# Optimization experiments

Measured on AMD Instinct MI355X. Metric: run time of the kernel, lower is better.

The kernel has to match this reference:

```python
import jax, jax.numpy as jnp
import numpy as np

NUM_HEADS = 12

def _elu1(x):
    return jax.nn.elu(x) + 1.0

def setup_inputs() -> dict:
    key = jax.random.key(0)
    ks = jax.random.split(key, 7)
    B, Nq, Nk, D = 8, 4096, 1024, 768
    s = 0.02
    return {
        "x_query": jax.random.normal(ks[0], (B, Nq, D), dtype=jnp.float32),
        "x_key_value": jax.random.normal(ks[1], (B, Nk, D), dtype=jnp.float32),
        "Wq": jax.random.normal(ks[2], (D, D), dtype=jnp.float32) * s,
        "Wk": jax.random.normal(ks[3], (D, D), dtype=jnp.float32) * s,
        "Wv": jax.random.normal(ks[4], (D, D), dtype=jnp.float32) * s,
        "Wo": jax.random.normal(ks[5], (D, D), dtype=jnp.float32) * s,
        "bo": jax.random.normal(ks[6], (D,), dtype=jnp.float32) * s,
    }

def reference(x_query, x_key_value, Wq, Wk, Wv, Wo, bo):
    B, Nq, D = x_query.shape
    Nk = x_key_value.shape[1]
    H = NUM_HEADS
    hd = D // H
    # projections (torch Linear: x @ W.T), split heads -> [B, H, N, hd]
    q = (x_query @ Wq.T).reshape(B, Nq, H, hd).transpose(0, 2, 1, 3)
    k = (x_key_value @ Wk.T).reshape(B, Nk, H, hd).transpose(0, 2, 1, 3)
    v = (x_key_value @ Wv.T).reshape(B, Nk, H, hd).transpose(0, 2, 1, 3)
    q = _elu1(q)
    k = _elu1(k)
    # kv: [B,H,hd,hd]; k_sum: [B,H,hd]
    kv = jnp.einsum('bhnd,bhne->bhde', k, v)
    k_sum = k.sum(axis=2)
    z = 1.0 / (jnp.einsum('bhqd,bhd->bhq', q, k_sum) + 1e-6)  # [B,H,Nq]
    attn_out = jnp.einsum('bhqd,bhde->bhqe', q, kv) * z[..., None]
    attn_out = attn_out.transpose(0, 2, 1, 3).reshape(B, Nq, D)
    return attn_out @ Wo.T + bo
```

## Files before the change

kernel.cpp:

```cpp
#include <hip/hip_runtime.h>

typedef _Float16 half8_t __attribute__((ext_vector_type(8)));
typedef _Float16 half4_t __attribute__((ext_vector_type(4)));
typedef float    float4_t __attribute__((ext_vector_type(4)));

#define DIM 768

#define GLOAD16(g, l) __builtin_amdgcn_global_load_lds(                        \
    (const __attribute__((address_space(1))) void*)(g),                        \
    (__attribute__((address_space(3))) void*)(l), 16, 0, 0)

__global__ __launch_bounds__(256) void cast_f32_f16(const float* __restrict__ s,
                                                    _Float16* __restrict__ d, int n8)
{
    int i = blockIdx.x * 256 + threadIdx.x;
    if (i < n8) {
        float4_t f0 = *(const float4_t*)&s[(size_t)i * 8];
        float4_t f1 = *(const float4_t*)&s[(size_t)i * 8 + 4];
        half8_t h;
        #pragma unroll
        for (int e = 0; e < 4; ++e) { h[e] = (_Float16)f0[e]; h[e + 4] = (_Float16)f1[e]; }
        *(half8_t*)&d[(size_t)i * 8] = h;
    }
}

__global__ __launch_bounds__(256) void cast4_f32_f16(
    const float* __restrict__ s0, const float* __restrict__ s1,
    const float* __restrict__ s2, const float* __restrict__ s3,
    _Float16* __restrict__ d0, _Float16* __restrict__ d1,
    _Float16* __restrict__ d2, _Float16* __restrict__ d3)
{
    const float* s; _Float16* d;
    switch (blockIdx.y) {
        case 0: s = s0; d = d0; break;
        case 1: s = s1; d = d1; break;
        case 2: s = s2; d = d2; break;
        default: s = s3; d = d3; break;
    }
    int i = blockIdx.x * 256 + threadIdx.x;
    float4_t f0 = *(const float4_t*)&s[(size_t)i * 8];
    float4_t f1 = *(const float4_t*)&s[(size_t)i * 8 + 4];
    half8_t h;
    #pragma unroll
    for (int e = 0; e < 4; ++e) { h[e] = (_Float16)f0[e]; h[e + 4] = (_Float16)f1[e]; }
    *(half8_t*)&d[(size_t)i * 8] = h;
}

template<bool ELU, bool BIAS, bool OUT_F32>
__global__ __launch_bounds__(256) void gemm_h16(const _Float16* __restrict__ A,
                                                const _Float16* __restrict__ W,
                                                const float* __restrict__ bias,
                                                void* __restrict__ Ov)
{
    __shared__ __align__(16) _Float16 As[128 * 64];
    __shared__ __align__(16) _Float16 Bs[128 * 64];

    const int nwg = gridDim.x;
    const int cpx = nwg >> 3;
    const int bid = (blockIdx.x & 7) * cpx + (blockIdx.x >> 3);
    const int brow = bid / 6;
    const int bcol = bid - brow * 6;
    const int row0 = brow * 128, col0 = bcol * 128;

    const int tid  = threadIdx.x;
    const int w    = tid >> 6, lane = tid & 63;
    const int lr   = lane & 15;
    const int lkg  = lane >> 4;
    const int wm   = (w & 1) * 64;
    const int wn   = (w >> 1) * 64;

    const int sr = w * 8 + (lane >> 3);
    const int sc = (lane & 7) * 8;
    const _Float16* Ag = A + (size_t)(row0 + sr) * DIM + sc;
    const _Float16* Wg = W + (size_t)(col0 + sr) * DIM + sc;

    float4_t acc[4][4] = {};

    for (int k0 = 0; k0 < DIM; k0 += 64) {
        #pragma unroll
        for (int j = 0; j < 4; ++j)
            GLOAD16(Ag + k0 + j * 32 * DIM, &As[j * 2048 + w * 512]);
        #pragma unroll
        for (int j = 0; j < 4; ++j)
            GLOAD16(Wg + k0 + j * 32 * DIM, &Bs[j * 2048 + w * 512]);
        __syncthreads();

        half8_t aF[2][4], bF[2][4];
        #pragma unroll
        for (int kk = 0; kk < 2; ++kk) {
            #pragma unroll
            for (int mi = 0; mi < 4; ++mi)
                aF[kk][mi] = *(const half8_t*)&As[(wm + mi * 16 + lr) * 64 + kk * 32 + lkg * 8];
            #pragma unroll
            for (int ni = 0; ni < 4; ++ni)
                bF[kk][ni] = *(const half8_t*)&Bs[(wn + ni * 16 + lr) * 64 + kk * 32 + lkg * 8];
        }
        #pragma unroll
        for (int kk = 0; kk < 2; ++kk)
            #pragma unroll
            for (int mi = 0; mi < 4; ++mi)
                #pragma unroll
                for (int ni = 0; ni < 4; ++ni)
                    acc[mi][ni] = __builtin_amdgcn_mfma_f32_16x16x32_f16(
                        aF[kk][mi], bF[kk][ni], acc[mi][ni], 0, 0, 0);
        __syncthreads();
    }

    #pragma unroll
    for (int mi = 0; mi < 4; ++mi) {
        #pragma unroll
        for (int ni = 0; ni < 4; ++ni) {
            #pragma unroll
            for (int e = 0; e < 4; ++e) {
                int r = row0 + wm + mi * 16 + lkg * 4 + e;
                int c = col0 + wn + ni * 16 + lr;
                float v = acc[mi][ni][e];
                if (ELU) v = (v > 0.0f) ? (v + 1.0f) : __expf(v);
                if (BIAS) v += bias[c];
                if (OUT_F32) ((float*)Ov)[(size_t)r * DIM + c] = v;
                else         ((_Float16*)Ov)[(size_t)r * DIM + c] = (_Float16)v;
            }
        }
    }
}

__global__ __launch_bounds__(256) void kv_reduce(const _Float16* __restrict__ k16,
                                                 const _Float16* __restrict__ v16,
                                                 float* __restrict__ kvh,
                                                 float* __restrict__ ksum)
{
    __shared__ __align__(16) _Float16 K[128][64];
    __shared__ __align__(16) _Float16 V[128][64];
    const int chunk = blockIdx.x;
    const int bh    = blockIdx.y;
    const int b = bh / 12, h = bh % 12;
    const int tid = threadIdx.x;

    const size_t base = ((size_t)b * 1024 + (size_t)chunk * 128) * DIM + h * 64;
    #pragma unroll
    for (int j = 0; j < 4; ++j) {
        int idx = j * 256 + tid;
        int r = idx >> 3, c = (idx & 7) * 8;
        *(half8_t*)&K[r][c] = *(const half8_t*)&k16[base + (size_t)r * DIM + c];
        *(half8_t*)&V[r][c] = *(const half8_t*)&v16[base + (size_t)r * DIM + c];
    }
    __syncthreads();

    const int d0 = (tid & 15) * 4;
    const int e0 = (tid >> 4) * 4;
    float acc[4][4] = {};
    #pragma unroll 4
    for (int n = 0; n < 128; ++n) {
        half4_t kd = *(const half4_t*)&K[n][d0];
        half4_t ve = *(const half4_t*)&V[n][e0];
        #pragma unroll
        for (int i = 0; i < 4; ++i)
            #pragma unroll
            for (int j = 0; j < 4; ++j)
                acc[i][j] += (float)ve[i] * (float)kd[j];
    }
    float* kvp = kvh + (size_t)bh * 64 * 64;
    #pragma unroll
    for (int i = 0; i < 4; ++i)
        #pragma unroll
        for (int j = 0; j < 4; ++j)
            atomicAdd(&kvp[(e0 + i) * 64 + d0 + j], acc[i][j]);

    if (tid < 64) {
        float s = 0.0f;
        for (int n = 0; n < 128; ++n) s += (float)K[n][tid];
        atomicAdd(&ksum[bh * 64 + tid], s);
    }
}

__global__ __launch_bounds__(256) void attn_kernel(_Float16* __restrict__ q16,
                                                   const float* __restrict__ kvh,
                                                   const float* __restrict__ ksum)
{
    __shared__ __align__(16) _Float16 Q[128][72];
    __shared__ __align__(16) _Float16 Bv[64][72];
    __shared__ float S[64];
    __shared__ float Z[128];

    const int h    = blockIdx.x;
    const int rb   = blockIdx.y;
    const int row0 = rb * 128;
    const int b    = row0 >> 12;
    const int bh   = b * 12 + h;
    const int tid  = threadIdx.x;

    #pragma unroll
    for (int j = 0; j < 4; ++j) {
        int idx = j * 256 + tid;
        int r = idx >> 3, c = (idx & 7) * 8;
        *(half8_t*)&Q[r][c] =
            *(const half8_t*)&q16[(size_t)(row0 + r) * DIM + h * 64 + c];
    }
    #pragma unroll
    for (int j = 0; j < 4; ++j) {
        int idx = j * 256 + tid;
        int r = idx >> 4, c = (idx & 15) * 4;
        float4_t f = *(const float4_t*)&kvh[((size_t)bh * 64 + r) * 64 + c];
        half4_t hh;
        #pragma unroll
        for (int e = 0; e < 4; ++e) hh[e] = (_Float16)f[e];
        *(half4_t*)&Bv[r][c] = hh;
    }
    if (tid < 64) S[tid] = ksum[bh * 64 + tid];
    __syncthreads();

    if (tid < 128) {
        float dot = 0.0f;
        #pragma unroll 8
        for (int d = 0; d < 64; ++d) dot += (float)Q[tid][d] * S[d];
        Z[tid] = 1.0f / (dot + 1e-6f);
    }
    __syncthreads();

    const int w = tid >> 6, lane = tid & 63;
    const int lr = lane & 15, lkg = lane >> 4;
    float4_t acc[2][4] = {};
    #pragma unroll
    for (int kc = 0; kc < 2; ++kc) {
        half8_t aF[2], bF[4];
        #pragma unroll
        for (int mi = 0; mi < 2; ++mi)
            aF[mi] = *(const half8_t*)&Q[w * 32 + mi * 16 + lr][kc * 32 + lkg * 8];
        #pragma unroll
        for (int ni = 0; ni < 4; ++ni)
            bF[ni] = *(const half8_t*)&Bv[ni * 16 + lr][kc * 32 + lkg * 8];
        #pragma unroll
        for (int mi = 0; mi < 2; ++mi)
            #pragma unroll
            for (int ni = 0; ni < 4; ++ni)
                acc[mi][ni] = __builtin_amdgcn_mfma_f32_16x16x32_f16(
                    aF[mi], bF[ni], acc[mi][ni], 0, 0, 0);
    }
    #pragma unroll
    for (int mi = 0; mi < 2; ++mi) {
        #pragma unroll
        for (int ni = 0; ni < 4; ++ni) {
            #pragma unroll
            for (int e = 0; e < 4; ++e) {
                int r = w * 32 + mi * 16 + lkg * 4 + e;
                float v = acc[mi][ni][e] * Z[r];
                q16[(size_t)(row0 + r) * DIM + h * 64 + ni * 16 + lr] = (_Float16)v;
            }
        }
    }
}

extern "C" void kernel_launch(void* const* d_in, const int* in_sizes, int n_in,
                              void* d_out, int out_size, void* d_ws, size_t ws_size,
                              hipStream_t stream)
{
    const float* xq  = (const float*)d_in[0];
    const float* xkv = (const float*)d_in[1];
    const float* Wq  = (const float*)d_in[2];
    const float* Wk  = (const float*)d_in[3];
    const float* Wv  = (const float*)d_in[4];
    const float* Wo  = (const float*)d_in[5];
    const float* bo  = (const float*)d_in[6];

    char* ws = (char*)d_ws;
    const size_t SZ_XKV16 = (size_t)8192 * 768 * 2;
    const size_t SZ_Q16   = (size_t)32768 * 768 * 2;
    const size_t SZ_W16   = (size_t)768 * 768 * 2;
    const size_t SZ_KVH   = (size_t)96 * 64 * 64 * 4;
    const size_t SZ_KSUM  = (size_t)96 * 64 * 4;

    _Float16* xkv16 = (_Float16*)(ws);
    _Float16* q16   = (_Float16*)(ws + SZ_XKV16);
    _Float16* Wq16  = (_Float16*)(ws + SZ_XKV16 + SZ_Q16);
    _Float16* Wk16  = (_Float16*)(ws + SZ_XKV16 + SZ_Q16 + SZ_W16);
    _Float16* Wv16  = (_Float16*)(ws + SZ_XKV16 + SZ_Q16 + 2 * SZ_W16);
    _Float16* Wo16  = (_Float16*)(ws + SZ_XKV16 + SZ_Q16 + 3 * SZ_W16);
    float*    kvh   = (float*)   (ws + SZ_XKV16 + SZ_Q16 + 4 * SZ_W16);
    float*    ksum  = (float*)   (ws + SZ_XKV16 + SZ_Q16 + 4 * SZ_W16 + SZ_KVH);

    char* ob = (char*)d_out;
    _Float16* xq16 = (_Float16*)(ob);
    _Float16* k16  = (_Float16*)(ob + 50331648);
    _Float16* v16  = (_Float16*)(ob + 50331648 + 12582912);
    float*    out  = (float*)d_out;

    cast_f32_f16<<<12288, 256, 0, stream>>>(xq,  xq16,  3145728);
    cast_f32_f16<<< 3072, 256, 0, stream>>>(xkv, xkv16,  786432);
    cast4_f32_f16<<<dim3(288, 4), 256, 0, stream>>>(Wq, Wk, Wv, Wo,
                                                    Wq16, Wk16, Wv16, Wo16);
    hipMemsetAsync(kvh, 0, SZ_KVH + SZ_KSUM, stream);

    gemm_h16<true , false, false><<< 384, 256, 0, stream>>>(xkv16, Wk16, nullptr, k16);
    gemm_h16<false, false, false><<< 384, 256, 0, stream>>>(xkv16, Wv16, nullptr, v16);
    gemm_h16<true , false, false><<<1536, 256, 0, stream>>>(xq16 , Wq16, nullptr, q16);

    kv_reduce<<<dim3(8, 96), 256, 0, stream>>>(k16, v16, kvh, ksum);
    attn_kernel<<<dim3(12, 256), 256, 0, stream>>>(q16, kvh, ksum);

    gemm_h16<false, true , true ><<<1536, 256, 0, stream>>>(q16, Wo16, bo, out);
}
```

Baseline: 253.8 us.

## Replace GEMM with 256x128-tile triple-buffered pipelined kernel using swizzled LDS

The fp16 MFMA GEMM moves from 128x128 tiles with 256 threads and a single LDS buffer to 256x128 tiles with 512 threads. Global-to-LDS loads run through a 3-stage ring prefetched two k-steps ahead. LDS addresses use an XOR swizzle to avoid bank conflicts, and split-phase barriers with s_setprio let MFMA work overlap the issue of the next loads. The aim is to hide global load latency and raise MFMA utilisation, at the cost of 144KB of LDS per block (one block per CU) and fewer blocks in the grid.

```diff
diff --git a/kernel.cpp b/kernel.cpp
--- a/kernel.cpp
+++ b/kernel.cpp
@@ -9,6 +9,8 @@
 #define GLOAD16(g, l) __builtin_amdgcn_global_load_lds(                        \
     (const __attribute__((address_space(1))) void*)(g),                        \
     (__attribute__((address_space(3))) void*)(l), 16, 0, 0)
+
+#define MFMA16(a, b, c) __builtin_amdgcn_mfma_f32_16x16x32_f16((a), (b), (c), 0, 0, 0)
 
 __global__ __launch_bounds__(256) void cast_f32_f16(const float* __restrict__ s,
                                                     _Float16* __restrict__ d, int n8)
@@ -47,73 +49,124 @@
 }
 
 template<bool ELU, bool BIAS, bool OUT_F32>
-__global__ __launch_bounds__(256) void gemm_h16(const _Float16* __restrict__ A,
-                                                const _Float16* __restrict__ W,
-                                                const float* __restrict__ bias,
-                                                void* __restrict__ Ov)
-{
-    __shared__ __align__(16) _Float16 As[128 * 64];
-    __shared__ __align__(16) _Float16 Bs[128 * 64];
+__global__ __launch_bounds__(512) void gemm256(const _Float16* __restrict__ A,
+                                               const _Float16* __restrict__ W,
+                                               const float* __restrict__ bias,
+                                               void* __restrict__ Ov)
+{
+    __shared__ __align__(16) _Float16 lds[3 * 24576];
 
     const int nwg = gridDim.x;
     const int cpx = nwg >> 3;
     const int bid = (blockIdx.x & 7) * cpx + (blockIdx.x >> 3);
-    const int brow = bid / 6;
-    const int bcol = bid - brow * 6;
-    const int row0 = brow * 128, col0 = bcol * 128;
+    const int brow = bid / 6, bcol = bid - brow * 6;
+    const int row0 = brow * 256, col0 = bcol * 128;
 
     const int tid  = threadIdx.x;
-    const int w    = tid >> 6, lane = tid & 63;
+    const int wid  = tid >> 6, lane = tid & 63;
+    const int wr   = wid >> 2;
+    const int wc   = wid & 3;
     const int lr   = lane & 15;
     const int lkg  = lane >> 4;
-    const int wm   = (w & 1) * 64;
-    const int wn   = (w >> 1) * 64;
-
-    const int sr = w * 8 + (lane >> 3);
-    const int sc = (lane & 7) * 8;
-    const _Float16* Ag = A + (size_t)(row0 + sr) * DIM + sc;
-    const _Float16* Wg = W + (size_t)(col0 + sr) * DIM + sc;
-
-    float4_t acc[4][4] = {};
-
-    for (int k0 = 0; k0 < DIM; k0 += 64) {
-        #pragma unroll
-        for (int j = 0; j < 4; ++j)
-            GLOAD16(Ag + k0 + j * 32 * DIM, &As[j * 2048 + w * 512]);
-        #pragma unroll
-        for (int j = 0; j < 4; ++j)
-            GLOAD16(Wg + k0 + j * 32 * DIM, &Bs[j * 2048 + w * 512]);
-        __syncthreads();
-
-        half8_t aF[2][4], bF[2][4];
-        #pragma unroll
-        for (int kk = 0; kk < 2; ++kk) {
-            #pragma unroll
-            for (int mi = 0; mi < 4; ++mi)
-                aF[kk][mi] = *(const half8_t*)&As[(wm + mi * 16 + lr) * 64 + kk * 32 + lkg * 8];
-            #pragma unroll
-            for (int ni = 0; ni < 4; ++ni)
-                bF[kk][ni] = *(const half8_t*)&Bs[(wn + ni * 16 + lr) * 64 + kk * 32 + lkg * 8];
-        }
-        #pragma unroll
-        for (int kk = 0; kk < 2; ++kk)
-            #pragma unroll
-            for (int mi = 0; mi < 4; ++mi)
-                #pragma unroll
-                for (int ni = 0; ni < 4; ++ni)
-                    acc[mi][ni] = __builtin_amdgcn_mfma_f32_16x16x32_f16(
-                        aF[kk][mi], bF[kk][ni], acc[mi][ni], 0, 0, 0);
-        __syncthreads();
-    }
-
-    #pragma unroll
-    for (int mi = 0; mi < 4; ++mi) {
-        #pragma unroll
-        for (int ni = 0; ni < 4; ++ni) {
+    const int x    = lr & 7;
+
+    const int  srow = wid * 8 + (lane >> 3);
+    const int  sg   = ((lane & 7) ^ (lane >> 3)) * 8;
+    const _Float16* Ast = A + (size_t)(row0 + srow) * DIM + sg;
+    const _Float16* Bst = W + (size_t)(col0 + srow) * DIM + sg;
+
+#define LDSA(s) (&lds[(s) * 24576])
+#define LDSB(s) (&lds[(s) * 24576 + 16384])
+#define STAGE_A(t, s, j) GLOAD16(Ast + (size_t)(t) * 64 + (size_t)(j) * 64 * DIM, \
+                                 LDSA(s) + (j) * 4096 + wid * 512)
+#define STAGE_B(t, s, j) GLOAD16(Bst + (size_t)(t) * 64 + (size_t)(j) * 64 * DIM, \
+                                 LDSB(s) + (j) * 4096 + wid * 512)
+
+    const int ard = (wr * 128 + lr) * 64;
+    const int brd = (wc * 32 + lr) * 64;
+    const int g0  = (lkg ^ x) * 8;
+    const int g1  = g0 ^ 32;
+
+    float4_t acc[8][2] = {};
+
+    STAGE_A(0, 0, 0); STAGE_A(0, 0, 1); STAGE_A(0, 0, 2); STAGE_A(0, 0, 3);
+    STAGE_B(0, 0, 0); STAGE_B(0, 0, 1);
+    STAGE_A(1, 1, 0); STAGE_A(1, 1, 1); STAGE_A(1, 1, 2); STAGE_A(1, 1, 3);
+    STAGE_B(1, 1, 0); STAGE_B(1, 1, 1);
+    asm volatile("s_waitcnt vmcnt(6)" ::: "memory");
+    __builtin_amdgcn_s_barrier();
+
+    int s = 0, s2 = 2;
+    for (int t = 0; t < 12; ++t) {
+        const _Float16* Asl = LDSA(s);
+        const _Float16* Bsl = LDSB(s);
+        const bool pf = (t < 10);
+
+        half8_t bf[2][2];
+        bf[0][0] = *(const half8_t*)&Bsl[brd + g0];
+        bf[0][1] = *(const half8_t*)&Bsl[brd + g1];
+        bf[1][0] = *(const half8_t*)&Bsl[brd + 1024 + g0];
+        bf[1][1] = *(const half8_t*)&Bsl[brd + 1024 + g1];
+        half8_t af0[4][2];
+        #pragma unroll
+        for (int i = 0; i < 4; ++i) {
+            af0[i][0] = *(const half8_t*)&Asl[ard + i * 1024 + g0];
+            af0[i][1] = *(const half8_t*)&Asl[ard + i * 1024 + g1];
+        }
+        if (pf) { STAGE_A(t + 2, s2, 0); STAGE_A(t + 2, s2, 1); STAGE_A(t + 2, s2, 2); }
+        __builtin_amdgcn_s_barrier();
+        asm volatile("s_waitcnt lgkmcnt(0)" ::: "memory");
+        __builtin_amdgcn_sched_barrier(0);
+        __builtin_amdgcn_s_setprio(1);
+        #pragma unroll
+        for (int i = 0; i < 4; ++i)
+            #pragma unroll
+            for (int ni = 0; ni < 2; ++ni) {
+                acc[i][ni] = MFMA16(af0[i][0], bf[ni][0], acc[i][ni]);
+                acc[i][ni] = MFMA16(af0[i][1], bf[ni][1], acc[i][ni]);
+            }
+        __builtin_amdgcn_s_setprio(0);
+        __builtin_amdgcn_sched_barrier(0);
+        __builtin_amdgcn_s_barrier();
+
+        half8_t af1[4][2];
+        #pragma unroll
+        for (int i = 0; i < 4; ++i) {
+            af1[i][0] = *(const half8_t*)&Asl[ard + 4096 + i * 1024 + g0];
+            af1[i][1] = *(const half8_t*)&Asl[ard + 4096 + i * 1024 + g1];
+        }
+        if (pf) { STAGE_A(t + 2, s2, 3); STAGE_B(t + 2, s2, 0); STAGE_B(t + 2, s2, 1); }
+        __builtin_amdgcn_s_barrier();
+        asm volatile("s_waitcnt lgkmcnt(0)" ::: "memory");
+        __builtin_amdgcn_sched_barrier(0);
+        __builtin_amdgcn_s_setprio(1);
+        #pragma unroll
+        for (int i = 0; i < 4; ++i)
+            #pragma unroll
+            for (int ni = 0; ni < 2; ++ni) {
+                acc[4 + i][ni] = MFMA16(af1[i][0], bf[ni][0], acc[4 + i][ni]);
+                acc[4 + i][ni] = MFMA16(af1[i][1], bf[ni][1], acc[4 + i][ni]);
+            }
+        __builtin_amdgcn_s_setprio(0);
+        __builtin_amdgcn_sched_barrier(0);
+
+        if (t < 11) {
+            if (pf) asm volatile("s_waitcnt vmcnt(6)" ::: "memory");
+            else    asm volatile("s_waitcnt vmcnt(0)" ::: "memory");
+            __builtin_amdgcn_s_barrier();
+        }
+        s  = (s  == 2) ? 0 : s  + 1;
+        s2 = (s2 == 2) ? 0 : s2 + 1;
+    }
+
+    #pragma unroll
+    for (int mi = 0; mi < 8; ++mi) {
+        #pragma unroll
+        for (int ni = 0; ni < 2; ++ni) {
             #pragma unroll
             for (int e = 0; e < 4; ++e) {
-                int r = row0 + wm + mi * 16 + lkg * 4 + e;
-                int c = col0 + wn + ni * 16 + lr;
+                int r = row0 + wr * 128 + mi * 16 + lkg * 4 + e;
+                int c = col0 + wc * 32 + ni * 16 + lr;
                 float v = acc[mi][ni][e];
                 if (ELU) v = (v > 0.0f) ? (v + 1.0f) : __expf(v);
                 if (BIAS) v += bias[c];
@@ -122,6 +175,10 @@
             }
         }
     }
+#undef LDSA
+#undef LDSB
+#undef STAGE_A
+#undef STAGE_B
 }
 
 __global__ __launch_bounds__(256) void kv_reduce(const _Float16* __restrict__ k16,
@@ -233,8 +290,7 @@
         for (int mi = 0; mi < 2; ++mi)
             #pragma unroll
             for (int ni = 0; ni < 4; ++ni)
-                acc[mi][ni] = __builtin_amdgcn_mfma_f32_16x16x32_f16(
-                    aF[mi], bF[ni], acc[mi][ni], 0, 0, 0);
+                acc[mi][ni] = MFMA16(aF[mi], bF[ni], acc[mi][ni]);
     }
     #pragma unroll
     for (int mi = 0; mi < 2; ++mi) {
@@ -290,12 +346,12 @@
                                                     Wq16, Wk16, Wv16, Wo16);
     hipMemsetAsync(kvh, 0, SZ_KVH + SZ_KSUM, stream);
 
-    gemm_h16<true , false, false><<< 384, 256, 0, stream>>>(xkv16, Wk16, nullptr, k16);
-    gemm_h16<false, false, false><<< 384, 256, 0, stream>>>(xkv16, Wv16, nullptr, v16);
-    gemm_h16<true , false, false><<<1536, 256, 0, stream>>>(xq16 , Wq16, nullptr, q16);
+    gemm256<true , false, false><<< 192, 512, 0, stream>>>(xkv16, Wk16, nullptr, k16);
+    gemm256<false, false, false><<< 192, 512, 0, stream>>>(xkv16, Wv16, nullptr, v16);
+    gemm256<true , false, false><<< 768, 512, 0, stream>>>(xq16 , Wq16, nullptr, q16);
 
     kv_reduce<<<dim3(8, 96), 256, 0, stream>>>(k16, v16, kvh, ksum);
     attn_kernel<<<dim3(12, 256), 256, 0, stream>>>(q16, kvh, ksum);
 
-    gemm_h16<false, true , true ><<<1536, 256, 0, stream>>>(q16, Wo16, bo, out);
-}
+    gemm256<false, true , true ><<< 768, 512, 0, stream>>>(q16, Wo16, bo, out);
+}
```

After: 230.6 us. -9.1%, faster.

## Pipeline GEMMs with triple-buffered LDS and fuse Q/K/V projections into one launch

Applied to the files above, without the earlier changes.

Replaces the single-buffered 128x128 GEMM with a 256x128-tile, 512-thread core that uses a three-stage global-to-LDS pipeline with k-steps of 32. It uses partial vmcnt waits, raw barriers and raised wave priority around the MFMA block. The three Q/K/V projection launches merge into one grid that dispatches by block id. The aim is to overlap global loads with MFMA work, cut barrier stalls and launch count, and improve tile reuse. In exchange, LDS use per block rises, and correctness now depends on hand-written waitcnt and sched-barrier ordering.

```diff
diff --git a/kernel.cpp b/kernel.cpp
--- a/kernel.cpp
+++ b/kernel.cpp
@@ -9,6 +9,8 @@
 #define GLOAD16(g, l) __builtin_amdgcn_global_load_lds(                        \
     (const __attribute__((address_space(1))) void*)(g),                        \
     (__attribute__((address_space(3))) void*)(l), 16, 0, 0)
+
+#define MFMA16(a, b, c) __builtin_amdgcn_mfma_f32_16x16x32_f16((a), (b), (c), 0, 0, 0)
 
 __global__ __launch_bounds__(256) void cast_f32_f16(const float* __restrict__ s,
                                                     _Float16* __restrict__ d, int n8)
@@ -46,79 +48,143 @@
     *(half8_t*)&d[(size_t)i * 8] = h;
 }
 
-template<bool ELU, bool BIAS, bool OUT_F32>
-__global__ __launch_bounds__(256) void gemm_h16(const _Float16* __restrict__ A,
-                                                const _Float16* __restrict__ W,
-                                                const float* __restrict__ bias,
-                                                void* __restrict__ Ov)
-{
-    __shared__ __align__(16) _Float16 As[128 * 64];
-    __shared__ __align__(16) _Float16 Bs[128 * 64];
-
-    const int nwg = gridDim.x;
-    const int cpx = nwg >> 3;
-    const int bid = (blockIdx.x & 7) * cpx + (blockIdx.x >> 3);
-    const int brow = bid / 6;
-    const int bcol = bid - brow * 6;
-    const int row0 = brow * 128, col0 = bcol * 128;
-
+__device__ __forceinline__ void gemm_core(const _Float16* __restrict__ A,
+                                          const _Float16* __restrict__ W,
+                                          int row0, int col0, _Float16* lds,
+                                          float4_t acc[4][4])
+{
     const int tid  = threadIdx.x;
-    const int w    = tid >> 6, lane = tid & 63;
-    const int lr   = lane & 15;
-    const int lkg  = lane >> 4;
-    const int wm   = (w & 1) * 64;
-    const int wn   = (w >> 1) * 64;
-
-    const int sr = w * 8 + (lane >> 3);
-    const int sc = (lane & 7) * 8;
-    const _Float16* Ag = A + (size_t)(row0 + sr) * DIM + sc;
-    const _Float16* Wg = W + (size_t)(col0 + sr) * DIM + sc;
+    const int wid  = tid >> 6, lane = tid & 63;
+    const int wr   = wid >> 1;
+    const int wc   = wid & 1;
+
+    const int srow  = lane & 15;
+    const int skoct = lane >> 4;
+    const _Float16* As0 = A + (size_t)(row0 + wid * 32 + srow)      * DIM + skoct * 8;
+    const _Float16* As1 = A + (size_t)(row0 + wid * 32 + 16 + srow) * DIM + skoct * 8;
+    const _Float16* Bs0 = W + (size_t)(col0 + wid * 16 + srow)      * DIM + skoct * 8;
+
+#define STAGE(t, s) do {                                                      \
+        GLOAD16(As0 + (t) * 32, &lds[(s) * 12288 + (2 * wid) * 512]);         \
+        GLOAD16(As1 + (t) * 32, &lds[(s) * 12288 + (2 * wid + 1) * 512]);     \
+        GLOAD16(Bs0 + (t) * 32, &lds[(s) * 12288 + 8192 + wid * 512]);        \
+    } while (0)
+
+    const int aoff = (wr * 4) * 512 + lane * 8;
+    const int boff = 8192 + (wc * 4) * 512 + lane * 8;
+
+    STAGE(0, 0);
+    STAGE(1, 1);
+    asm volatile("s_waitcnt vmcnt(3)" ::: "memory");
+    __builtin_amdgcn_s_barrier();
+    __builtin_amdgcn_sched_barrier(0);
+
+    int s = 0, s2 = 2;
+    for (int t = 0; t < 24; ++t) {
+        const _Float16* sl = &lds[s * 12288];
+        half8_t af[4], bf[4];
+        #pragma unroll
+        for (int mi = 0; mi < 4; ++mi)
+            af[mi] = *(const half8_t*)&sl[aoff + mi * 512];
+        #pragma unroll
+        for (int ni = 0; ni < 4; ++ni)
+            bf[ni] = *(const half8_t*)&sl[boff + ni * 512];
+        if (t < 22) STAGE(t + 2, s2);
+
+        __builtin_amdgcn_s_setprio(1);
+        #pragma unroll
+        for (int mi = 0; mi < 4; ++mi)
+            #pragma unroll
+            for (int ni = 0; ni < 4; ++ni)
+                acc[mi][ni] = MFMA16(af[mi], bf[ni], acc[mi][ni]);
+        __builtin_amdgcn_s_setprio(0);
+
+        if (t < 23) {
+            __builtin_amdgcn_sched_barrier(0);
+            if (t < 22) asm volatile("s_waitcnt vmcnt(3)" ::: "memory");
+            else        asm volatile("s_waitcnt vmcnt(0)" ::: "memory");
+            __builtin_amdgcn_s_barrier();
+            __builtin_amdgcn_sched_barrier(0);
+        }
+        s  = (s  == 2) ? 0 : s  + 1;
+        s2 = (s2 == 2) ? 0 : s2 + 1;
+    }
+#undef STAGE
+}
+
+__global__ __launch_bounds__(512, 4) void proj_qkv(
+    const _Float16* __restrict__ xq16, const _Float16* __restrict__ xkv16,
+    const _Float16* __restrict__ Wq16, const _Float16* __restrict__ Wk16,
+    const _Float16* __restrict__ Wv16,
+    _Float16* __restrict__ q16, _Float16* __restrict__ k16,
+    _Float16* __restrict__ v16)
+{
+    __shared__ __align__(16) _Float16 lds[3 * 12288];
+
+    const int cpx = gridDim.x >> 3;
+    int bid = (blockIdx.x & 7) * cpx + (blockIdx.x >> 3);
+
+    const _Float16 *A, *W;
+    _Float16 *O;
+    bool elu;
+    int brow, bcol;
+    if (bid < 768) {
+        A = xq16; W = Wq16; O = q16; elu = true;
+        brow = bid / 6; bcol = bid - brow * 6;
+    } else {
+        int u = bid - 768;
+        int mat = u / 192;  u -= mat * 192;
+        A = xkv16; W = mat ? Wv16 : Wk16; O = mat ? v16 : k16; elu = !mat;
+        brow = u / 6; bcol = u - brow * 6;
+    }
+    const int row0 = brow * 256, col0 = bcol * 128;
 
     float4_t acc[4][4] = {};
-
-    for (int k0 = 0; k0 < DIM; k0 += 64) {
-        #pragma unroll
-        for (int j = 0; j < 4; ++j)
-            GLOAD16(Ag + k0 + j * 32 * DIM, &As[j * 2048 + w * 512]);
-        #pragma unroll
-        for (int j = 0; j < 4; ++j)
-            GLOAD16(Wg + k0 + j * 32 * DIM, &Bs[j * 2048 + w * 512]);
-        __syncthreads();
-
-        half8_t aF[2][4], bF[2][4];
-        #pragma unroll
-        for (int kk = 0; kk < 2; ++kk) {
-            #pragma unroll
-            for (int mi = 0; mi < 4; ++mi)
-                aF[kk][mi] = *(const half8_t*)&As[(wm + mi * 16 + lr) * 64 + kk * 32 + lkg * 8];
-            #pragma unroll
-            for (int ni = 0; ni < 4; ++ni)
-                bF[kk][ni] = *(const half8_t*)&Bs[(wn + ni * 16 + lr) * 64 + kk * 32 + lkg * 8];
+    gemm_core(A, W, row0, col0, lds, acc);
+
+    const int wid = threadIdx.x >> 6, lane = threadIdx.x & 63;
+    const int wr = wid >> 1, wc = wid & 1, lr = lane & 15, lkg = lane >> 4;
+    #pragma unroll
+    for (int mi = 0; mi < 4; ++mi) {
+        #pragma unroll
+        for (int ni = 0; ni < 4; ++ni) {
+            #pragma unroll
+            for (int e = 0; e < 4; ++e) {
+                int r = row0 + wr * 64 + mi * 16 + lkg * 4 + e;
+                int c = col0 + wc * 64 + ni * 16 + lr;
+                float v = acc[mi][ni][e];
+                if (elu) v = (v > 0.0f) ? (v + 1.0f) : __expf(v);
+                O[(size_t)r * DIM + c] = (_Float16)v;
+            }
         }
-        #pragma unroll
-        for (int kk = 0; kk < 2; ++kk)
-            #pragma unroll
-            for (int mi = 0; mi < 4; ++mi)
-                #pragma unroll
-                for (int ni = 0; ni < 4; ++ni)
-                    acc[mi][ni] = __builtin_amdgcn_mfma_f32_16x16x32_f16(
-                        aF[kk][mi], bF[kk][ni], acc[mi][ni], 0, 0, 0);
-        __syncthreads();
-    }
-
+    }
+}
+
+__global__ __launch_bounds__(512, 4) void out_proj(
+    const _Float16* __restrict__ a16, const _Float16* __restrict__ Wo16,
+    const float* __restrict__ bo, float* __restrict__ out)
+{
+    __shared__ __align__(16) _Float16 lds[3 * 12288];
+
+    const int cpx = gridDim.x >> 3;
+    int bid = (blockIdx.x & 7) * cpx + (blockIdx.x >> 3);
+    const int brow = bid / 6, bcol = bid - brow * 6;
+    const int row0 = brow * 256, col0 = bcol * 128;
+
+    float4_t acc[4][4] = {};
+    gemm_core(a16, Wo16, row0, col0, lds, acc);
+
+    const int wid = threadIdx.x >> 6, lane = threadIdx.x & 63;
+    const int wr = wid >> 1, wc = wid & 1, lr = lane & 15, lkg = lane >> 4;
     #pragma unroll
     for (int mi = 0; mi < 4; ++mi) {
         #pragma unroll
         for (int ni = 0; ni < 4; ++ni) {
             #pragma unroll
             for (int e = 0; e < 4; ++e) {
-                int r = row0 + wm + mi * 16 + lkg * 4 + e;
-                int c = col0 + wn + ni * 16 + lr;
-                float v = acc[mi][ni][e];
-                if (ELU) v = (v > 0.0f) ? (v + 1.0f) : __expf(v);
-                if (BIAS) v += bias[c];
-                if (OUT_F32) ((float*)Ov)[(size_t)r * DIM + c] = v;
-                else         ((_Float16*)Ov)[(size_t)r * DIM + c] = (_Float16)v;
+                int r = row0 + wr * 64 + mi * 16 + lkg * 4 + e;
+                int c = col0 + wc * 64 + ni * 16 + lr;
+                out[(size_t)r * DIM + c] = acc[mi][ni][e] + bo[c];
             }
         }
     }
@@ -233,8 +299,7 @@
         for (int mi = 0; mi < 2; ++mi)
             #pragma unroll
             for (int ni = 0; ni < 4; ++ni)
-                acc[mi][ni] = __builtin_amdgcn_mfma_f32_16x16x32_f16(
-                    aF[mi], bF[ni], acc[mi][ni], 0, 0, 0);
+                acc[mi][ni] = MFMA16(aF[mi], bF[ni], acc[mi][ni]);
     }
     #pragma unroll
     for (int mi = 0; mi < 2; ++mi) {
@@ -290,12 +355,11 @@
                                                     Wq16, Wk16, Wv16, Wo16);
     hipMemsetAsync(kvh, 0, SZ_KVH + SZ_KSUM, stream);
 
-    gemm_h16<true , false, false><<< 384, 256, 0, stream>>>(xkv16, Wk16, nullptr, k16);
-    gemm_h16<false, false, false><<< 384, 256, 0, stream>>>(xkv16, Wv16, nullptr, v16);
-    gemm_h16<true , false, false><<<1536, 256, 0, stream>>>(xq16 , Wq16, nullptr, q16);
+    proj_qkv<<<1152, 512, 0, stream>>>(xq16, xkv16, Wq16, Wk16, Wv16,
+                                       q16, k16, v16);
 
     kv_reduce<<<dim3(8, 96), 256, 0, stream>>>(k16, v16, kvh, ksum);
     attn_kernel<<<dim3(12, 256), 256, 0, stream>>>(q16, kvh, ksum);
 
-    gemm_h16<false, true , true ><<<1536, 256, 0, stream>>>(q16, Wo16, bo, out);
-}
+    out_proj<<<768, 512, 0, stream>>>(q16, Wo16, bo, out);
+}
```

Result: slower. 259.9 us (+2.4%).
